# Kernel tuning notes

Measured on AMD Instinct MI355X. Metric: run time of the kernel, lower is better.

Reference implementation:

```python
import jax, jax.numpy as jnp
import numpy as np

H, D = 2, 128            # heads, per-head dim
F_OUT = H * D            # out_channels = 256
N_ADD = 20000
N_DEL = 20000
E = 200000
N_SEL = 4096


def setup_inputs() -> dict:
    key = jax.random.key(0)
    ks = jax.random.split(key, 24)
    p = lambda k, shp: (jax.random.normal(k, shp, dtype=jnp.float32) * 0.05)
    inp = {
        "x_add": jax.random.normal(ks[0], (N_ADD, 768), dtype=jnp.float32),
        "x_del": jax.random.normal(ks[1], (N_DEL, 768), dtype=jnp.float32),
        # per-node-type projections (torch Linear: W [out,in], b [out])
        "W_add": p(ks[2], (F_OUT, 768)), "b_add": p(ks[3], (F_OUT,)),
        "W_del": p(ks[4], (F_OUT, 768)), "b_del": p(ks[5], (F_OUT,)),
        # per-edge-type attention vectors [H, D]
        "att_ad_s": p(ks[6], (H, D)), "att_ad_d": p(ks[7], (H, D)),
        "att_da_s": p(ks[8], (H, D)), "att_da_d": p(ks[9], (H, D)),
        "att_aa_s": p(ks[10], (H, D)), "att_aa_d": p(ks[11], (H, D)),
        "att_dd_s": p(ks[12], (H, D)), "att_dd_d": p(ks[13], (H, D)),
        # semantic attention: k_lin Linear(F_OUT->F_OUT) and query q [F_OUT]
        "k_W": p(ks[14], (F_OUT, F_OUT)), "k_b": p(ks[15], (F_OUT,)),
        "q": p(ks[16], (F_OUT,)),
        # edge indices: row 0 = src node ids, row 1 = dst node ids
        "ei_ad": jax.random.randint(ks[17], (2, E), 0, N_ADD),
        "ei_da": jax.random.randint(ks[18], (2, E), 0, N_DEL),
        "ei_aa": jax.random.randint(ks[19], (2, E), 0, N_ADD),
        "ei_dd": jax.random.randint(ks[20], (2, E), 0, N_DEL),
        "del_idx": jax.random.randint(ks[21], (N_SEL,), 0, N_DEL),
    }
    return inp


def _seg_softmax(a, seg, n):
    # numerically-stable softmax over edges grouped by destination node
    m = jax.ops.segment_max(a, seg, num_segments=n)
    m = jnp.where(jnp.isfinite(m), m, 0.0)
    e = jnp.exp(a - m[seg])
    s = jax.ops.segment_sum(e, seg, num_segments=n)
    return e / (s[seg] + 1e-16)


def _edge_attn(x_src, x_dst, att_s, att_d, ei, n_dst):
    # x_*: [N, H, D]; GAT-style additive attention with leaky_relu(0.2)
    a_s = (x_src * att_s).sum(-1)                   # [Ns, H]
    a_d = (x_dst * att_d).sum(-1)                   # [Nd, H]
    alpha = jax.nn.leaky_relu(a_s[ei[0]] + a_d[ei[1]], 0.2)  # [E, H]
    alpha = _seg_softmax(alpha, ei[1], n_dst)       # [E, H]
    msg = x_src[ei[0]] * alpha[:, :, None]          # [E, H, D]
    out = jax.ops.segment_sum(msg, ei[1], num_segments=n_dst)  # [Nd, H, D]
    return jax.nn.relu(out).reshape(n_dst, F_OUT)


def _group(xs, q, k_W, k_b):
    # semantic (metapath-level) attention
    out = jnp.stack(xs)                              # [M, N, F]
    score = (q * jnp.tanh(out @ k_W.T + k_b).mean(axis=1)).sum(-1)  # [M]
    attn = jax.nn.softmax(score)
    return (attn[:, None, None] * out).sum(0)        # [N, F]


def reference(x_add, x_del, W_add, b_add, W_del, b_del,
              att_ad_s, att_ad_d, att_da_s, att_da_d,
              att_aa_s, att_aa_d, att_dd_s, att_dd_d,
              k_W, k_b, q, ei_ad, ei_da, ei_aa, ei_dd, del_idx):
    ha = (x_add @ W_add.T + b_add).reshape(N_ADD, H, D)
    hd = (x_del @ W_del.T + b_del).reshape(N_DEL, H, D)
    # messages grouped by destination node type
    out_del_ad = _edge_attn(ha, hd, att_ad_s, att_ad_d, ei_ad, N_DEL)
    out_del_dd = _edge_attn(hd, hd, att_dd_s, att_dd_d, ei_dd, N_DEL)
    out_add_da = _edge_attn(hd, ha, att_da_s, att_da_d, ei_da, N_ADD)
    out_add_aa = _edge_attn(ha, ha, att_aa_s, att_aa_d, ei_aa, N_ADD)
    out_del = _group([out_del_ad, out_del_dd], q, k_W, k_b)
    _ = _group([out_add_da, out_add_aa], q, k_W, k_b)  # computed by HANConv, unused downstream
    return out_del[del_idx]  # index_select on del_node
```

## Files before the change

kernel.cpp:

```cpp
#include <hip/hip_runtime.h>
#include <hip/hip_bf16.h>


typedef unsigned short u16;
typedef __attribute__((ext_vector_type(8))) __bf16 bf16x8;
typedef __attribute__((ext_vector_type(4))) float f32x4;
typedef const __attribute__((address_space(1))) unsigned int* gu32p;
typedef __attribute__((address_space(3))) unsigned int* su32p;

__device__ inline float bf2f(u16 u) {
    union { unsigned int i; float f; } c; c.i = ((unsigned int)u) << 16; return c.f;
}
__device__ inline u16 f2bf(float f) {
    union { float f; unsigned int i; } c; c.f = f;
    return (u16)((c.i + 0x7fffu + ((c.i >> 16) & 1u)) >> 16);
}
__device__ inline bf16x8 cvt8(f32x4 a, f32x4 b) {
    bf16x8 r;
    r[0] = (__bf16)a[0]; r[1] = (__bf16)a[1]; r[2] = (__bf16)a[2]; r[3] = (__bf16)a[3];
    r[4] = (__bf16)b[0]; r[5] = (__bf16)b[1]; r[6] = (__bf16)b[2]; r[7] = (__bf16)b[3];
    return r;
}
__device__ inline float fast_tanh(float x) {
    x = fminf(9.f, fmaxf(-9.f, x));
    float t = __expf(2.f * x);
    return (t - 1.f) / (t + 1.f);
}

__global__ __launch_bounds__(256) void prep_count(const float* __restrict__ W0, u16* __restrict__ wb0,
                                                  const float* __restrict__ W1, u16* __restrict__ wb1,
                                                  const float* __restrict__ kW, u16* __restrict__ kwb,
                                                  const int* __restrict__ eiA, int* __restrict__ cntA,
                                                  const int* __restrict__ eiB, int* __restrict__ cntB, int E) {
    int b = blockIdx.x;
    if (b < 224) {
        int idx = b * 256 + threadIdx.x;
        const float* s; u16* d; int i;
        if (idx < 24576)      { s = W0; d = wb0; i = idx; }
        else if (idx < 49152) { s = W1; d = wb1; i = idx - 24576; }
        else                  { s = kW; d = kwb; i = idx - 49152; }
        int e = i * 8;
        *(bf16x8*)(d + e) = cvt8(*(const f32x4*)(s + e), *(const f32x4*)(s + e + 4));
    } else {
        int idx = (b - 224) * 256 + threadIdx.x;
        int which = idx >= E;
        int e = idx - (which ? E : 0);
        if (e >= E) return;
        const int* ei = which ? eiB : eiA;
        int* cnt = which ? cntB : cntA;
        atomicAdd(&cnt[ei[E + e]], 1);
    }
}

__global__ __launch_bounds__(512, 4) void gemm_h3(
    const float* __restrict__ X0, const u16* __restrict__ Wb0,
    const float* __restrict__ b0, u16* __restrict__ H0,
    const float* __restrict__ X1, const u16* __restrict__ Wb1,
    const float* __restrict__ b1, u16* __restrict__ H1,
    const float* __restrict__ w_ads, const float* __restrict__ w_add,
    const float* __restrict__ w_dds, const float* __restrict__ w_ddd,
    float* __restrict__ as_ad, float* __restrict__ ad_ad,
    float* __restrict__ as_dd, float* __restrict__ ad_dd, int M) {
    __shared__ u16 lds[40960];
    int id = blockIdx.x;
    int which = id >= 313;
    int bm = which ? id - 313 : id;
    const float* X = which ? X1 : X0;
    const u16* Wb = which ? Wb1 : Wb0;
    const float* bias = which ? b1 : b0;
    u16* H = which ? H1 : H0;

    int tid = threadIdx.x;
    int w = tid >> 6, lane = tid & 63;
    int wrow = w & 1, wcol = w >> 1;
    int row16 = lane & 15, quad = lane >> 4;

#define ISSUE_B(kt, slot) { \
    _Pragma("unroll") \
    for (int j = 0; j < 2; ++j) { \
        int rloc = (w * 2 + j) * 16 + (lane >> 2); \
        int cc = (lane & 3) ^ ((rloc >> 1) & 3); \
        const u16* gp = Wb + (size_t)rloc * 768 + (kt) * 32 + cc * 8; \
        u16* lp = lds + 16384 + (slot) * 8192 + (w * 2 + j) * 512; \
        __builtin_amdgcn_global_load_lds((gu32p)(const void*)gp, (su32p)(void*)lp, 16, 0, 0); \
    } }

#define ALOAD(c, ar) { \
    _Pragma("unroll") \
    for (int i = 0; i < 4; ++i) { \
        int idx = i * 512 + tid; \
        int row = idx >> 5, col4 = idx & 31; \
        int rg = bm * 64 + row; if (rg > M - 1) rg = M - 1; \
        ar[i] = *(const f32x4*)(X + (size_t)rg * 768 + (c) * 128 + col4 * 4); \
    } }

#define AWRITE(c, ar) { \
    _Pragma("unroll") \
    for (int i = 0; i < 4; ++i) { \
        int idx = i * 512 + tid; \
        int row = idx >> 5, col4 = idx & 31; \
        int off = ((c) & 1) * 8192 + row * 128 + (((col4 >> 1) ^ (row & 7)) << 3) + ((col4 & 1) << 2); \
        ushort4 v; v.x = f2bf(ar[i][0]); v.y = f2bf(ar[i][1]); v.z = f2bf(ar[i][2]); v.w = f2bf(ar[i][3]); \
        *(ushort4*)(lds + off) = v; \
    } }

#define STEP(ks) { \
    const int ksl = (ks) & 3, buf = ((ks) >> 2) & 1, slot = (ks) % 3; \
    bf16x8 af[2], bv[4]; \
    _Pragma("unroll") \
    for (int mi = 0; mi < 2; ++mi) { \
        int r = wrow * 32 + mi * 16 + row16; \
        af[mi] = *(const bf16x8*)(lds + buf * 8192 + r * 128 + (((ksl * 4 + quad) ^ (r & 7)) << 3)); \
    } \
    _Pragma("unroll") \
    for (int ni = 0; ni < 4; ++ni) { \
        int r = wcol * 64 + ni * 16 + row16; \
        bv[ni] = *(const bf16x8*)(lds + 16384 + slot * 8192 + r * 32 + ((quad ^ ((r >> 1) & 3)) << 3)); \
    } \
    _Pragma("unroll") \
    for (int mi = 0; mi < 2; ++mi) \
        _Pragma("unroll") \
        for (int ni = 0; ni < 4; ++ni) \
            acc[mi][ni] = __builtin_amdgcn_mfma_f32_16x16x32_bf16(af[mi], bv[ni], acc[mi][ni], 0, 0, 0); \
}

    f32x4 a0[4], a1[4];
    ISSUE_B(0, 0)
    ISSUE_B(1, 1)
    ALOAD(0, a0)
    ALOAD(1, a1)
    asm volatile("s_waitcnt vmcnt(4)" ::: "memory");
    AWRITE(0, a0)
    asm volatile("s_waitcnt lgkmcnt(0)" ::: "memory");
    asm volatile("s_barrier" ::: "memory");

    f32x4 acc[2][4] = {};
#pragma unroll
    for (int ks = 0; ks < 24; ++ks) {
        if (ks > 0) {
            const int wv = (ks == 23) ? 0 : (ks >= 17) ? 2 : ((ks & 2) ? 6 : 2);
            if (wv == 0)      asm volatile("s_waitcnt vmcnt(0) lgkmcnt(0)" ::: "memory");
            else if (wv == 2) asm volatile("s_waitcnt vmcnt(2) lgkmcnt(0)" ::: "memory");
            else              asm volatile("s_waitcnt vmcnt(6) lgkmcnt(0)" ::: "memory");
            asm volatile("s_barrier" ::: "memory");
        }
        if (ks < 22) ISSUE_B(ks + 2, (ks + 2) % 3)
        if (ks == 0) {
            asm volatile("s_waitcnt vmcnt(2)" ::: "memory");
            AWRITE(1, a1)
        } else if ((ks & 3) == 0 && ks <= 16) {
            AWRITE(ks / 4 + 1, a0)
        }
        if ((ks & 3) == 1 && ks <= 13) ALOAD(ks / 4 + 2, a0)
        STEP(ks)
    }
#undef ISSUE_B
#undef ALOAD
#undef AWRITE
#undef STEP

    __syncthreads();
    u16* eps = lds;
    const int SE2 = 264;
#pragma unroll
    for (int mi = 0; mi < 2; ++mi)
#pragma unroll
        for (int ni = 0; ni < 4; ++ni) {
            int col = wcol * 64 + ni * 16 + row16;
            float bvv = bias[col];
#pragma unroll
            for (int r = 0; r < 4; ++r)
                eps[(wrow * 32 + mi * 16 + quad * 4 + r) * SE2 + col] = f2bf(acc[mi][ni][r] + bvv);
        }
    __syncthreads();
    int mlim = M - bm * 64;
    int c0 = (tid & 31) * 8;
    int hh = c0 >> 7;
    float wv0[8], wv1[8], wv2[8];
    const float* att0 = which ? w_add : w_ads;
#pragma unroll
    for (int j = 0; j < 8; ++j) {
        wv0[j] = att0[c0 + j];
        wv1[j] = w_dds[c0 + j];
        wv2[j] = w_ddd[c0 + j];
    }
#pragma unroll
    for (int p = 0; p < 4; ++p) {
        int row = p * 16 + (tid >> 5);
        union { uint4 q; u16 s[8]; } v;
        v.q = *(const uint4*)(eps + row * SE2 + c0);
        if (row < mlim)
            *(uint4*)(H + (size_t)(bm * 64 + row) * 256 + c0) = v.q;
        float d0 = 0.f, d1 = 0.f, d2 = 0.f;
#pragma unroll
        for (int j = 0; j < 8; ++j) {
            float hv = bf2f(v.s[j]);
            d0 += hv * wv0[j];
            if (which) { d1 += hv * wv1[j]; d2 += hv * wv2[j]; }
        }
#pragma unroll
        for (int off = 8; off >= 1; off >>= 1) {
            d0 += __shfl_down(d0, off, 16);
            if (which) { d1 += __shfl_down(d1, off, 16); d2 += __shfl_down(d2, off, 16); }
        }
        if ((tid & 15) == 0 && row < mlim) {
            int n = bm * 64 + row;
            if (!which) {
                unsafeAtomicAdd(&as_ad[n * 2 + hh], d0);
            } else {
                unsafeAtomicAdd(&ad_ad[n * 2 + hh], d0);
                unsafeAtomicAdd(&as_dd[n * 2 + hh], d1);
                unsafeAtomicAdd(&ad_dd[n * 2 + hh], d2);
            }
        }
    }
}

__global__ __launch_bounds__(1024) void scan_two(const int* __restrict__ cntA, int* __restrict__ offA,
                                                 const int* __restrict__ cntB, int* __restrict__ offB, int n) {
    const int* cnt = blockIdx.x ? cntB : cntA;
    int* off = blockIdx.x ? offB : offA;
    __shared__ int wsum[16];
    __shared__ int woff[16];
    __shared__ int tot_s;
    __shared__ int carry_s;
    int tid = threadIdx.x, wid = tid >> 6, lane = tid & 63;
    if (tid == 0) carry_s = 0;
    __syncthreads();
    for (int base = 0; base < n; base += 4096) {
        int i = base + tid * 4;
        int v0 = (i + 0 < n) ? cnt[i + 0] : 0;
        int v1 = (i + 1 < n) ? cnt[i + 1] : 0;
        int v2 = (i + 2 < n) ? cnt[i + 2] : 0;
        int v3 = (i + 3 < n) ? cnt[i + 3] : 0;
        int s0 = v0, s1 = s0 + v1, s2 = s1 + v2, s3 = s2 + v3;
        int x = s3;
#pragma unroll
        for (int d = 1; d < 64; d <<= 1) {
            int t = __shfl_up(x, d, 64);
            if (lane >= d) x += t;
        }
        if (lane == 63) wsum[wid] = x;
        __syncthreads();
        if (wid == 0) {
            int s = (lane < 16) ? wsum[lane] : 0;
#pragma unroll
            for (int d = 1; d < 16; d <<= 1) {
                int t = __shfl_up(s, d, 64);
                if (lane >= d) s += t;
            }
            if (lane < 16) woff[lane] = s - wsum[lane];
            if (lane == 15) tot_s = s;
        }
        __syncthreads();
        int basev = carry_s + woff[wid] + (x - s3);
        if (i + 0 < n) off[i + 0] = basev;
        if (i + 1 < n) off[i + 1] = basev + s0;
        if (i + 2 < n) off[i + 2] = basev + s1;
        if (i + 3 < n) off[i + 3] = basev + s2;
        __syncthreads();
        if (tid == 0) carry_s += tot_s;
    }
    __syncthreads();
    if (tid == 0) off[n] = carry_s;
}

__global__ __launch_bounds__(256) void fill_csr2(const int* __restrict__ eiA, const int* __restrict__ offA,
                                                 int* __restrict__ curA, int* __restrict__ srcsA,
                                                 const int* __restrict__ eiB, const int* __restrict__ offB,
                                                 int* __restrict__ curB, int* __restrict__ srcsB, int E) {
    int idx = blockIdx.x * 256 + threadIdx.x;
    int which = idx >= E;
    int e = idx - (which ? E : 0);
    if (e >= E) return;
    const int* ei = which ? eiB : eiA;
    const int* off = which ? offB : offA;
    int* cursor = which ? curB : curA;
    int* srcs = which ? srcsB : srcsA;
    int s = ei[e], d = ei[E + e];
    int slot = off[d] + atomicAdd(&cursor[d], 1);
    srcs[slot] = s;
}

__global__ __launch_bounds__(256) void edge_gather2(const int* __restrict__ offA, const int* __restrict__ srcsA,
                                                    const float* __restrict__ asA, const float* __restrict__ adA,
                                                    const u16* __restrict__ hA, u16* __restrict__ outA,
                                                    const int* __restrict__ offB, const int* __restrict__ srcsB,
                                                    const float* __restrict__ asB, const float* __restrict__ adB,
                                                    const u16* __restrict__ hB, u16* __restrict__ outB, int N) {
    int gid = blockIdx.x * 256 + threadIdx.x;
    int dall = gid >> 6;
    int which = dall >= N;
    int d = dall - (which ? N : 0);
    if (d >= N) return;
    const int* off = which ? offB : offA;
    const int* srcs = which ? srcsB : srcsA;
    const float* a_src = which ? asB : asA;
    const float* a_dst = which ? adB : adA;
    const u16* h = which ? hB : hA;
    u16* out = which ? outB : outA;
    int lane = gid & 63;
    int hh = lane >> 5;
    int f = lane * 4;
    float ad0 = a_dst[d * 2 + hh];
    int beg = off[d], end = off[d + 1];
    float4 acc = {0.f, 0.f, 0.f, 0.f};
    float S = 0.f;
    int p = beg;
    for (; p + 2 <= end; p += 2) {
        int s0 = srcs[p], s1 = srcs[p + 1];
        ushort4 x0 = *(const ushort4*)(h + (size_t)s0 * 256 + f);
        ushort4 x1 = *(const ushort4*)(h + (size_t)s1 * 256 + f);
        float v0 = a_src[s0 * 2 + hh] + ad0;
        float v1 = a_src[s1 * 2 + hh] + ad0;
        v0 = v0 > 0.f ? v0 : 0.2f * v0;
        v1 = v1 > 0.f ? v1 : 0.2f * v1;
        float e0 = __expf(v0), e1 = __expf(v1);
        S += e0 + e1;
        acc.x += e0 * bf2f(x0.x) + e1 * bf2f(x1.x);
        acc.y += e0 * bf2f(x0.y) + e1 * bf2f(x1.y);
        acc.z += e0 * bf2f(x0.z) + e1 * bf2f(x1.z);
        acc.w += e0 * bf2f(x0.w) + e1 * bf2f(x1.w);
    }
    if (p < end) {
        int s0 = srcs[p];
        ushort4 x0 = *(const ushort4*)(h + (size_t)s0 * 256 + f);
        float v0 = a_src[s0 * 2 + hh] + ad0;
        v0 = v0 > 0.f ? v0 : 0.2f * v0;
        float e0 = __expf(v0);
        S += e0;
        acc.x += e0 * bf2f(x0.x);
        acc.y += e0 * bf2f(x0.y);
        acc.z += e0 * bf2f(x0.z);
        acc.w += e0 * bf2f(x0.w);
    }
    float inv = 1.f / (S + 1e-16f);
    ushort4 o = {f2bf(acc.x * inv), f2bf(acc.y * inv), f2bf(acc.z * inv), f2bf(acc.w * inv)};
    *(ushort4*)(out + (size_t)d * 256 + f) = o;
}

#define SK 264
__global__ __launch_bounds__(256) void kgemm_score2(const u16* __restrict__ outA,
                                                    const u16* __restrict__ outB,
                                                    const u16* __restrict__ kwb,
                                                    const float* __restrict__ kb,
                                                    const float* __restrict__ qv,
                                                    float* __restrict__ score) {
    __shared__ u16 Bs[128 * SK];
    __shared__ float red[4];
    int slot = blockIdx.x >> 8;
    int b = blockIdx.x & 255;
    const u16* outm = slot ? outB : outA;
    int bn = b & 1;
    int bidx = b >> 1;
    int tid = threadIdx.x;
    int w = tid >> 6, lane = tid & 63;
    int row16 = lane & 15, quad = lane >> 4;

#pragma unroll
    for (int i = 0; i < 16; ++i) {
        int c = tid + 256 * i;
        int r = c >> 5, col8 = (c & 31) * 8;
        *(bf16x8*)(Bs + r * SK + col8) = *(const bf16x8*)(kwb + (size_t)(bn * 128 + r) * 256 + col8);
    }
    __syncthreads();

    float kb0 = kb[bn * 128 + w * 32 + row16];
    float qn0 = qv[bn * 128 + w * 32 + row16];
    float kb1 = kb[bn * 128 + w * 32 + 16 + row16];
    float qn1 = qv[bn * 128 + w * 32 + 16 + row16];
    const u16* b0 = Bs + (w * 32 + row16) * SK + quad * 8;
    const u16* b1 = Bs + (w * 32 + 16 + row16) * SK + quad * 8;

    union U { uint4 q; u16 s[8]; bf16x8 v; };
    float p = 0.f;
    for (int mt = bidx; mt < 1250; mt += 128) {
        const u16* arow = outm + (size_t)(mt * 16 + row16) * 256 + quad * 8;
        U a[8];
#pragma unroll
        for (int s8 = 0; s8 < 8; ++s8) a[s8].q = *(const uint4*)(arow + s8 * 32);
        f32x4 acc0 = {0.f,0.f,0.f,0.f}, acc1 = {0.f,0.f,0.f,0.f};
#pragma unroll
        for (int s8 = 0; s8 < 8; ++s8) {
#pragma unroll
            for (int j = 0; j < 8; ++j)
                if (a[s8].s[j] & 0x8000u) a[s8].s[j] = 0;
            bf16x8 bf0 = *(const bf16x8*)(b0 + s8 * 32);
            bf16x8 bf1 = *(const bf16x8*)(b1 + s8 * 32);
            acc0 = __builtin_amdgcn_mfma_f32_16x16x32_bf16(a[s8].v, bf0, acc0, 0, 0, 0);
            acc1 = __builtin_amdgcn_mfma_f32_16x16x32_bf16(a[s8].v, bf1, acc1, 0, 0, 0);
        }
#pragma unroll
        for (int r = 0; r < 4; ++r) {
            p += qn0 * fast_tanh(acc0[r] + kb0);
            p += qn1 * fast_tanh(acc1[r] + kb1);
        }
    }
#pragma unroll
    for (int off = 32; off >= 1; off >>= 1) p += __shfl_down(p, off, 64);
    if (lane == 0) red[w] = p;
    __syncthreads();
    if (tid == 0) unsafeAtomicAdd(&score[slot], red[0] + red[1] + red[2] + red[3]);
}

__global__ __launch_bounds__(256) void final_combine(const u16* __restrict__ out_ad,
                                                     const u16* __restrict__ out_dd,
                                                     const float* __restrict__ score,
                                                     const int* __restrict__ del_idx,
                                                     float* __restrict__ out) {
    int i = blockIdx.x;
    int f = threadIdx.x;
    int node = del_idx[i];
    float s0 = score[0] * (1.f / 20000.f);
    float s1 = score[1] * (1.f / 20000.f);
    float m = fmaxf(s0, s1);
    float e0 = __expf(s0 - m), e1 = __expf(s1 - m);
    float inv = 1.f / (e0 + e1);
    float a0 = e0 * inv, a1 = e1 * inv;
    float v0 = bf2f(out_ad[(size_t)node * 256 + f]); v0 = v0 > 0.f ? v0 : 0.f;
    float v1 = bf2f(out_dd[(size_t)node * 256 + f]); v1 = v1 > 0.f ? v1 : 0.f;
    out[(size_t)i * 256 + f] = a0 * v0 + a1 * v1;
}

extern "C" void kernel_launch(void* const* d_in, const int* in_sizes, int n_in,
                              void* d_out, int out_size, void* d_ws, size_t ws_size,
                              hipStream_t stream) {
    const float* x_add    = (const float*)d_in[0];
    const float* x_del    = (const float*)d_in[1];
    const float* W_add    = (const float*)d_in[2];
    const float* b_add    = (const float*)d_in[3];
    const float* W_del    = (const float*)d_in[4];
    const float* b_del    = (const float*)d_in[5];
    const float* att_ad_s = (const float*)d_in[6];
    const float* att_ad_d = (const float*)d_in[7];
    const float* att_dd_s = (const float*)d_in[12];
    const float* att_dd_d = (const float*)d_in[13];
    const float* k_W      = (const float*)d_in[14];
    const float* k_b      = (const float*)d_in[15];
    const float* q        = (const float*)d_in[16];
    const int* ei_ad      = (const int*)d_in[17];
    const int* ei_dd      = (const int*)d_in[20];
    const int* del_idx    = (const int*)d_in[21];
    float* out = (float*)d_out;

    const int N = 20000, E = 200000;
    char* ws = (char*)d_ws;
    size_t o = 0;
    int* cnt_ad = (int*)(ws + o); o += (size_t)N * 4;
    int* cur_ad = (int*)(ws + o); o += (size_t)N * 4;
    int* cnt_dd = (int*)(ws + o); o += (size_t)N * 4;
    int* cur_dd = (int*)(ws + o); o += (size_t)N * 4;
    float* as_ad = (float*)(ws + o); o += (size_t)N * 2 * 4;
    float* ad_ad = (float*)(ws + o); o += (size_t)N * 2 * 4;
    float* as_dd = (float*)(ws + o); o += (size_t)N * 2 * 4;
    float* ad_dd = (float*)(ws + o); o += (size_t)N * 2 * 4;
    float* score = (float*)(ws + o); o += 256;
    size_t zero_bytes = o;
    u16* wb_add = (u16*)(ws + o); o += (size_t)256 * 768 * 2;
    u16* wb_del = (u16*)(ws + o); o += (size_t)256 * 768 * 2;
    u16* kwb    = (u16*)(ws + o); o += (size_t)256 * 256 * 2;
    int* off_ad = (int*)(ws + o); o += (size_t)(N + 1) * 4;
    int* off_dd = (int*)(ws + o); o += (size_t)(N + 1) * 4;
    int* srcs_ad = (int*)(ws + o); o += (size_t)E * 4;
    int* srcs_dd = (int*)(ws + o); o += (size_t)E * 4;
    u16* out_ad = (u16*)(ws + o); o += (size_t)N * 256 * 2;
    u16* out_dd = (u16*)(ws + o); o += (size_t)N * 256 * 2;
    u16* ha    = (u16*)(ws + o); o += (size_t)N * 256 * 2;
    u16* hd    = (u16*)(ws + o); o += (size_t)N * 256 * 2;

    hipMemsetAsync(d_ws, 0, zero_bytes, stream);

    prep_count<<<224 + (2 * E + 255) / 256, 256, 0, stream>>>(
        W_add, wb_add, W_del, wb_del, k_W, kwb, ei_ad, cnt_ad, ei_dd, cnt_dd, E);
    scan_two<<<2, 1024, 0, stream>>>(cnt_ad, off_ad, cnt_dd, off_dd, N);
    fill_csr2<<<(2 * E + 255) / 256, 256, 0, stream>>>(ei_ad, off_ad, cur_ad, srcs_ad,
                                                       ei_dd, off_dd, cur_dd, srcs_dd, E);

    gemm_h3<<<626, 512, 0, stream>>>(x_add, wb_add, b_add, ha,
                                     x_del, wb_del, b_del, hd,
                                     att_ad_s, att_ad_d, att_dd_s, att_dd_d,
                                     as_ad, ad_ad, as_dd, ad_dd, N);

    edge_gather2<<<10000, 256, 0, stream>>>(off_ad, srcs_ad, as_ad, ad_ad, ha, out_ad,
                                            off_dd, srcs_dd, as_dd, ad_dd, hd, out_dd, N);

    kgemm_score2<<<512, 256, 0, stream>>>(out_ad, out_dd, kwb, k_b, q, score);
    final_combine<<<4096, 256, 0, stream>>>(out_ad, out_dd, score, del_idx, out);
}
```

Baseline: 329.3 us.

## Fold CSR fill into GEMM launch, widen edge gather, branchless ReLU mask

The CSR fill kernel is merged into the projection GEMM launch as extra blocks, so one launch goes away and the scatter can overlap the GEMM. The edge gather now uses 32 lanes per destination, each loading 8 bf16 values (16 bytes) with a 4-way unrolled edge loop, which halves the threads and raises memory-level parallelism per load. The per-element sign test that clamps negative bf16 values to zero in the k-GEMM becomes a branchless 32-bit mask. The extra fill blocks carry the GEMM's 40 KB LDS allocation and may crowd the GEMM blocks' occupancy.

```diff
diff --git a/kernel.cpp b/kernel.cpp
--- a/kernel.cpp
+++ b/kernel.cpp
@@ -52,7 +52,7 @@
     }
 }
 
-__global__ __launch_bounds__(512, 4) void gemm_h3(
+__global__ __launch_bounds__(512, 4) void gemm_fill(
     const float* __restrict__ X0, const u16* __restrict__ Wb0,
     const float* __restrict__ b0, u16* __restrict__ H0,
     const float* __restrict__ X1, const u16* __restrict__ Wb1,
@@ -60,8 +60,27 @@
     const float* __restrict__ w_ads, const float* __restrict__ w_add,
     const float* __restrict__ w_dds, const float* __restrict__ w_ddd,
     float* __restrict__ as_ad, float* __restrict__ ad_ad,
-    float* __restrict__ as_dd, float* __restrict__ ad_dd, int M) {
+    float* __restrict__ as_dd, float* __restrict__ ad_dd, int M,
+    const int* __restrict__ eiA, const int* __restrict__ offA,
+    int* __restrict__ curA, int* __restrict__ srcsA,
+    const int* __restrict__ eiB, const int* __restrict__ offB,
+    int* __restrict__ curB, int* __restrict__ srcsB, int E) {
     __shared__ u16 lds[40960];
+    if (blockIdx.x >= 626) {
+        int idx = (int)(blockIdx.x - 626) * 512 + threadIdx.x;
+        int whichE = idx >= E;
+        int e = idx - (whichE ? E : 0);
+        if (e < E) {
+            const int* ei = whichE ? eiB : eiA;
+            const int* off = whichE ? offB : offA;
+            int* cursor = whichE ? curB : curA;
+            int* srcs = whichE ? srcsB : srcsA;
+            int s = ei[e], d = ei[E + e];
+            int slot = off[d] + atomicAdd(&cursor[d], 1);
+            srcs[slot] = s;
+        }
+        return;
+    }
     int id = blockIdx.x;
     int which = id >= 313;
     int bm = which ? id - 313 : id;
@@ -265,33 +284,16 @@
     if (tid == 0) off[n] = carry_s;
 }
 
-__global__ __launch_bounds__(256) void fill_csr2(const int* __restrict__ eiA, const int* __restrict__ offA,
-                                                 int* __restrict__ curA, int* __restrict__ srcsA,
-                                                 const int* __restrict__ eiB, const int* __restrict__ offB,
-                                                 int* __restrict__ curB, int* __restrict__ srcsB, int E) {
-    int idx = blockIdx.x * 256 + threadIdx.x;
-    int which = idx >= E;
-    int e = idx - (which ? E : 0);
-    if (e >= E) return;
-    const int* ei = which ? eiB : eiA;
-    const int* off = which ? offB : offA;
-    int* cursor = which ? curB : curA;
-    int* srcs = which ? srcsB : srcsA;
-    int s = ei[e], d = ei[E + e];
-    int slot = off[d] + atomicAdd(&cursor[d], 1);
-    srcs[slot] = s;
-}
-
-__global__ __launch_bounds__(256) void edge_gather2(const int* __restrict__ offA, const int* __restrict__ srcsA,
+__global__ __launch_bounds__(256) void edge_gather3(const int* __restrict__ offA, const int* __restrict__ srcsA,
                                                     const float* __restrict__ asA, const float* __restrict__ adA,
                                                     const u16* __restrict__ hA, u16* __restrict__ outA,
                                                     const int* __restrict__ offB, const int* __restrict__ srcsB,
                                                     const float* __restrict__ asB, const float* __restrict__ adB,
                                                     const u16* __restrict__ hB, u16* __restrict__ outB, int N) {
     int gid = blockIdx.x * 256 + threadIdx.x;
-    int dall = gid >> 6;
-    int which = dall >= N;
-    int d = dall - (which ? N : 0);
+    int grp = gid >> 5;
+    int which = grp >= N;
+    int d = grp - (which ? N : 0);
     if (d >= N) return;
     const int* off = which ? offB : offA;
     const int* srcs = which ? srcsB : srcsA;
@@ -299,44 +301,51 @@
     const float* a_dst = which ? adB : adA;
     const u16* h = which ? hB : hA;
     u16* out = which ? outB : outA;
-    int lane = gid & 63;
-    int hh = lane >> 5;
-    int f = lane * 4;
+    int l = gid & 31;
+    int hh = l >> 4;
+    int f = l * 8;
     float ad0 = a_dst[d * 2 + hh];
     int beg = off[d], end = off[d + 1];
-    float4 acc = {0.f, 0.f, 0.f, 0.f};
+    float acc[8] = {0.f, 0.f, 0.f, 0.f, 0.f, 0.f, 0.f, 0.f};
     float S = 0.f;
+    union U8 { uint4 q; u16 s[8]; };
     int p = beg;
-    for (; p + 2 <= end; p += 2) {
-        int s0 = srcs[p], s1 = srcs[p + 1];
-        ushort4 x0 = *(const ushort4*)(h + (size_t)s0 * 256 + f);
-        ushort4 x1 = *(const ushort4*)(h + (size_t)s1 * 256 + f);
+    for (; p + 4 <= end; p += 4) {
+        int s0 = srcs[p], s1 = srcs[p + 1], s2 = srcs[p + 2], s3 = srcs[p + 3];
+        U8 x0, x1, x2, x3;
+        x0.q = *(const uint4*)(h + (size_t)s0 * 256 + f);
+        x1.q = *(const uint4*)(h + (size_t)s1 * 256 + f);
+        x2.q = *(const uint4*)(h + (size_t)s2 * 256 + f);
+        x3.q = *(const uint4*)(h + (size_t)s3 * 256 + f);
         float v0 = a_src[s0 * 2 + hh] + ad0;
         float v1 = a_src[s1 * 2 + hh] + ad0;
+        float v2 = a_src[s2 * 2 + hh] + ad0;
+        float v3 = a_src[s3 * 2 + hh] + ad0;
         v0 = v0 > 0.f ? v0 : 0.2f * v0;
         v1 = v1 > 0.f ? v1 : 0.2f * v1;
-        float e0 = __expf(v0), e1 = __expf(v1);
-        S += e0 + e1;
-        acc.x += e0 * bf2f(x0.x) + e1 * bf2f(x1.x);
-        acc.y += e0 * bf2f(x0.y) + e1 * bf2f(x1.y);
-        acc.z += e0 * bf2f(x0.z) + e1 * bf2f(x1.z);
-        acc.w += e0 * bf2f(x0.w) + e1 * bf2f(x1.w);
-    }
-    if (p < end) {
+        v2 = v2 > 0.f ? v2 : 0.2f * v2;
+        v3 = v3 > 0.f ? v3 : 0.2f * v3;
+        float e0 = __expf(v0), e1 = __expf(v1), e2 = __expf(v2), e3 = __expf(v3);
+        S += (e0 + e1) + (e2 + e3);
+#pragma unroll
+        for (int j = 0; j < 8; ++j)
+            acc[j] += e0 * bf2f(x0.s[j]) + e1 * bf2f(x1.s[j]) + e2 * bf2f(x2.s[j]) + e3 * bf2f(x3.s[j]);
+    }
+    for (; p < end; ++p) {
         int s0 = srcs[p];
-        ushort4 x0 = *(const ushort4*)(h + (size_t)s0 * 256 + f);
+        U8 x0; x0.q = *(const uint4*)(h + (size_t)s0 * 256 + f);
         float v0 = a_src[s0 * 2 + hh] + ad0;
         v0 = v0 > 0.f ? v0 : 0.2f * v0;
         float e0 = __expf(v0);
         S += e0;
-        acc.x += e0 * bf2f(x0.x);
-        acc.y += e0 * bf2f(x0.y);
-        acc.z += e0 * bf2f(x0.z);
-        acc.w += e0 * bf2f(x0.w);
+#pragma unroll
+        for (int j = 0; j < 8; ++j) acc[j] += e0 * bf2f(x0.s[j]);
     }
     float inv = 1.f / (S + 1e-16f);
-    ushort4 o = {f2bf(acc.x * inv), f2bf(acc.y * inv), f2bf(acc.z * inv), f2bf(acc.w * inv)};
-    *(ushort4*)(out + (size_t)d * 256 + f) = o;
+    union U8 o;
+#pragma unroll
+    for (int j = 0; j < 8; ++j) o.s[j] = f2bf(acc[j] * inv);
+    *(uint4*)(out + (size_t)d * 256 + f) = o.q;
 }
 
 #define SK 264
@@ -372,7 +381,7 @@
     const u16* b0 = Bs + (w * 32 + row16) * SK + quad * 8;
     const u16* b1 = Bs + (w * 32 + 16 + row16) * SK + quad * 8;
 
-    union U { uint4 q; u16 s[8]; bf16x8 v; };
+    union U { uint4 q; unsigned int u[4]; u16 s[8]; bf16x8 v; };
     float p = 0.f;
     for (int mt = bidx; mt < 1250; mt += 128) {
         const u16* arow = outm + (size_t)(mt * 16 + row16) * 256 + quad * 8;
@@ -383,8 +392,12 @@
 #pragma unroll
         for (int s8 = 0; s8 < 8; ++s8) {
 #pragma unroll
-            for (int j = 0; j < 8; ++j)
-                if (a[s8].s[j] & 0x8000u) a[s8].s[j] = 0;
+            for (int u = 0; u < 4; ++u) {
+                unsigned int x = a[s8].u[u];
+                unsigned int sg = x & 0x80008000u;
+                unsigned int m = sg | (sg - (sg >> 15));
+                a[s8].u[u] = x & ~m;
+            }
             bf16x8 bf0 = *(const bf16x8*)(b0 + s8 * 32);
             bf16x8 bf1 = *(const bf16x8*)(b1 + s8 * 32);
             acc0 = __builtin_amdgcn_mfma_f32_16x16x32_bf16(a[s8].v, bf0, acc0, 0, 0, 0);
@@ -473,16 +486,18 @@
     prep_count<<<224 + (2 * E + 255) / 256, 256, 0, stream>>>(
         W_add, wb_add, W_del, wb_del, k_W, kwb, ei_ad, cnt_ad, ei_dd, cnt_dd, E);
     scan_two<<<2, 1024, 0, stream>>>(cnt_ad, off_ad, cnt_dd, off_dd, N);
-    fill_csr2<<<(2 * E + 255) / 256, 256, 0, stream>>>(ei_ad, off_ad, cur_ad, srcs_ad,
-                                                       ei_dd, off_dd, cur_dd, srcs_dd, E);
-
-    gemm_h3<<<626, 512, 0, stream>>>(x_add, wb_add, b_add, ha,
-                                     x_del, wb_del, b_del, hd,
-                                     att_ad_s, att_ad_d, att_dd_s, att_dd_d,
-                                     as_ad, ad_ad, as_dd, ad_dd, N);
-
-    edge_gather2<<<10000, 256, 0, stream>>>(off_ad, srcs_ad, as_ad, ad_ad, ha, out_ad,
-                                            off_dd, srcs_dd, as_dd, ad_dd, hd, out_dd, N);
+
+    gemm_fill<<<626 + (2 * E + 511) / 512, 512, 0, stream>>>(
+        x_add, wb_add, b_add, ha,
+        x_del, wb_del, b_del, hd,
+        att_ad_s, att_ad_d, att_dd_s, att_dd_d,
+        as_ad, ad_ad, as_dd, ad_dd, N,
+        ei_ad, off_ad, cur_ad, srcs_ad,
+        ei_dd, off_dd, cur_dd, srcs_dd, E);
+
+    edge_gather3<<<(2 * N * 32 + 255) / 256, 256, 0, stream>>>(
+        off_ad, srcs_ad, as_ad, ad_ad, ha, out_ad,
+        off_dd, srcs_dd, as_dd, ad_dd, hd, out_dd, N);
 
     kgemm_score2<<<512, 256, 0, stream>>>(out_ad, out_dd, kwb, k_b, q, score);
     final_combine<<<4096, 256, 0, stream>>>(out_ad, out_dd, score, del_idx, out);
```

Measured after the change: 307.1 us. 6.7% less time.
